# Performance work log

Hardware: AMD Instinct MI355X
Metric: run time of the kernel (lower is better)

Reference implementation:

```python
import jax, jax.numpy as jnp
import numpy as np

EMBED_DIM = 1024
NUM_HEADS = 16
HEAD_DIM = EMBED_DIM // NUM_HEADS
SCALE = HEAD_DIM ** -0.5
B, S = 2, 2048


def setup_inputs() -> dict:
    key = jax.random.key(0)
    ks = jax.random.split(key, 11)
    lim = 1.0 / np.sqrt(EMBED_DIM)
    def lin(kw, kb):
        W = jax.random.uniform(kw, (EMBED_DIM, EMBED_DIM), jnp.float32, -lim, lim)
        b = jax.random.uniform(kb, (EMBED_DIM,), jnp.float32, -lim, lim)
        return W, b
    Wq, bq = lin(ks[0], ks[1])
    Wk, bk = lin(ks[2], ks[3])
    Wv, bv = lin(ks[4], ks[5])
    Wo, bo = lin(ks[6], ks[7])
    query = jax.random.normal(ks[8], (B, S, EMBED_DIM), jnp.float32)
    key_t = jax.random.normal(ks[9], (B, S, EMBED_DIM), jnp.float32)
    value = jax.random.normal(ks[10], (B, S, EMBED_DIM), jnp.float32)
    return {"query": query, "key": key_t, "value": value,
            "Wq": Wq, "bq": bq, "Wk": Wk, "bk": bk,
            "Wv": Wv, "bv": bv, "Wo": Wo, "bo": bo}


def reference(query, key, value, Wq, bq, Wk, bk, Wv, bv, Wo, bo):
    # 'flash' path with attn_mask=None == full softmax attention (chunking is
    # only an execution schedule; per-chunk softmax is over the full key axis).
    b, s, _ = query.shape
    def heads(x, W, bias):
        y = x @ W.T + bias                      # [b, s, E]
        return y.reshape(b, s, NUM_HEADS, HEAD_DIM).transpose(0, 2, 1, 3)  # [b, h, s, d]
    q = heads(query, Wq, bq)
    k = heads(key, Wk, bk)
    v = heads(value, Wv, bv)
    scores = jnp.einsum('bhqd,bhkd->bhqk', q, k) * SCALE
    attn = jax.nn.softmax(scores, axis=-1)
    out = jnp.einsum('bhqk,bhkd->bhqd', attn, v)
    out = out.transpose(0, 2, 1, 3).reshape(b, s, EMBED_DIM)
    return out @ Wo.T + bo
```

## Files before the change

### kernel.cpp

```cpp
#include <hip/hip_runtime.h>

typedef unsigned short u16;
typedef unsigned int u32;
typedef __attribute__((ext_vector_type(8))) __bf16 bf16x8;
typedef __attribute__((ext_vector_type(4))) float f32x4;
typedef __attribute__((ext_vector_type(16))) float f32x16;
typedef __attribute__((ext_vector_type(4))) unsigned short u16x4;
typedef __attribute__((ext_vector_type(8))) unsigned short u16x8;
typedef __attribute__((ext_vector_type(4))) unsigned int u32x4;

#define DEV static __device__ __forceinline__

DEV void async_copy16(const void* g, void* l) {
  __builtin_amdgcn_global_load_lds((const __attribute__((address_space(1))) void*)g,
                                   (__attribute__((address_space(3))) void*)l, 16, 0, 0);
}
DEV float b2f(u16 s) { union { unsigned u; float f; } v; v.u = ((unsigned)s) << 16; return v.f; }
DEV u16 f2b(float f) {
  union { float f; unsigned u; } v; v.f = f;
  unsigned r = v.u + 0x7FFFu + ((v.u >> 16) & 1u);
  return (u16)(r >> 16);
}
DEV u32 pack2bf(float a, float b) {
  u32 ua = __float_as_uint(a) + 0x8000u;
  u32 ub = __float_as_uint(b) + 0x8000u;
  return __builtin_amdgcn_perm(ub, ua, 0x07060302u);
}
DEV int wave_detect_bf16(const unsigned* q, int lane) {
  const unsigned w = q[lane & 63];
  const unsigned e = (w >> 7) & 0xFFu;
  const bool inr = (e >= 100u && e <= 132u);
  return (__popcll(__ballot(inr)) >= 48) ? 1 : 0;
}

#define MFMA(a, b, c) __builtin_amdgcn_mfma_f32_16x16x32_bf16((a), (b), (c), 0, 0, 0)
#define MFMA32(a, b, c) __builtin_amdgcn_mfma_f32_32x32x16_bf16((a), (b), (c), 0, 0, 0)

__global__ void convert_inputs(
    const void* s0, const void* s1, const void* s2,
    const void* s3, const void* s4, const void* s5, const void* s6,
    const void* s7, const void* s8, const void* s9, const void* s10,
    u16* __restrict__ d0, u16* __restrict__ d1, u16* __restrict__ d2,
    u16* __restrict__ d3, u16* __restrict__ d4, u16* __restrict__ d5, u16* __restrict__ d6,
    float* __restrict__ e7, float* __restrict__ e8, float* __restrict__ e9, float* __restrict__ e10)
{
  const int bi = blockIdx.y;
  const void* src = nullptr; u16* db = nullptr; float* df = nullptr; int n = 0;
  switch (bi) {
    case 0:  src = s0;  db = d0; n = 4194304; break;
    case 1:  src = s1;  db = d1; n = 4194304; break;
    case 2:  src = s2;  db = d2; n = 4194304; break;
    case 3:  src = s3;  db = d3; n = 1048576; break;
    case 4:  src = s4;  db = d4; n = 1048576; break;
    case 5:  src = s5;  db = d5; n = 1048576; break;
    case 6:  src = s6;  db = d6; n = 1048576; break;
    case 7:  src = s7;  df = e7; n = 1024; break;
    case 8:  src = s8;  df = e8; n = 1024; break;
    case 9:  src = s9;  df = e9; n = 1024; break;
    default: src = s10; df = e10; n = 1024; break;
  }
  const int isbf = wave_detect_bf16((const unsigned*)s0, threadIdx.x);
  const int stride = gridDim.x * 256 * 8;
  for (int i = (blockIdx.x * 256 + threadIdx.x) * 8; i < n; i += stride) {
    if (db) {
      u16x8 v;
      if (isbf) {
        v = *(const u16x8*)((const u16*)src + i);
      } else {
        const f32x4* sf = (const f32x4*)((const float*)src + i);
        const f32x4 x0 = sf[0], x1 = sf[1];
#pragma unroll
        for (int j = 0; j < 4; ++j) { v[j] = f2b(x0[j]); v[4 + j] = f2b(x1[j]); }
      }
      *(u16x8*)(db + i) = v;
    } else {
#pragma unroll
      for (int j = 0; j < 8; ++j) {
        float x = isbf ? b2f(((const u16*)src)[i + j]) : ((const float*)src)[i + j];
        df[i + j] = x;
      }
    }
  }
}

__global__ __launch_bounds__(256, 3)
void gemm_qkv(const u16* __restrict__ X0, const u16* __restrict__ X1, const u16* __restrict__ X2,
              const u16* __restrict__ W0, const u16* __restrict__ W1, const u16* __restrict__ W2,
              const float* __restrict__ B0, const float* __restrict__ B1, const float* __restrict__ B2,
              u16* __restrict__ Y0, u16* __restrict__ Y1, u16* __restrict__ Y2,
              float* __restrict__ Yf, const unsigned* __restrict__ qdet, int mode0)
{
  __shared__ __align__(16) u16 smem[17408];
  u16* As = smem;
  u16* Bs = smem + 8192;

  const int z = blockIdx.z;
  const u16* X  = (z == 0) ? X0 : ((z == 1) ? X1 : X2);
  const u16* W  = (z == 0) ? W0 : ((z == 1) ? W1 : W2);
  const float* Bi = (z == 0) ? B0 : ((z == 1) ? B1 : B2);
  u16* Y        = (z == 0) ? Y0 : ((z == 1) ? Y1 : Y2);
  const int mode = mode0 ? mode0 : z;

  const int t = threadIdx.x, wave = t >> 6, lane = t & 63;
  const int lane15 = lane & 15, quad = lane >> 4, l7 = lane15 & 7;
  const int m0 = blockIdx.y * 128, n0 = blockIdx.x * 128;

  const int srow = lane >> 3;
  const int schunk = (lane & 7) ^ srow;
  const u16* gA = X + (size_t)(m0 + wave * 32 + srow) * 1024 + schunk * 8;
  const u16* gB = W + (size_t)(n0 + wave * 32 + srow) * 1024 + schunk * 8;
  u16* lA = &As[wave * 32 * 64];
  u16* lB = &Bs[wave * 32 * 64];

  f32x4 acc[4][4];
#pragma unroll
  for (int i = 0; i < 4; ++i)
#pragma unroll
    for (int j = 0; j < 4; ++j) acc[i][j] = (f32x4){0.f, 0.f, 0.f, 0.f};

  const int wr = wave >> 1, wc = wave & 1;

  for (int k0 = 0; k0 < 1024; k0 += 64) {
#pragma unroll
    for (int r = 0; r < 4; ++r) async_copy16(gA + (size_t)r * 8 * 1024, lA + r * 8 * 64);
#pragma unroll
    for (int r = 0; r < 4; ++r) async_copy16(gB + (size_t)r * 8 * 1024, lB + r * 8 * 64);
    gA += 64; gB += 64;
    __syncthreads();

#pragma unroll
    for (int kk = 0; kk < 2; ++kk) {
      bf16x8 af[4], bfv[4];
#pragma unroll
      for (int mt = 0; mt < 4; ++mt)
        af[mt] = *(const bf16x8*)&As[(wr * 64 + mt * 16 + lane15) * 64 + ((kk * 4 + quad) ^ l7) * 8];
#pragma unroll
      for (int nt = 0; nt < 4; ++nt)
        bfv[nt] = *(const bf16x8*)&Bs[(wc * 64 + nt * 16 + lane15) * 64 + ((kk * 4 + quad) ^ l7) * 8];
#pragma unroll
      for (int mt = 0; mt < 4; ++mt)
#pragma unroll
        for (int nt = 0; nt < 4; ++nt)
          acc[mt][nt] = MFMA(af[mt], bfv[nt], acc[mt][nt]);
    }
    __syncthreads();
  }

  const float qscale = 0.125f * 1.44269504088896340736f;

  if (mode == 2) {
    u16* T2 = smem;
    __syncthreads();
#pragma unroll
    for (int mt = 0; mt < 4; ++mt) {
      const int sl_base = wr * 64 + mt * 16 + quad * 4;
#pragma unroll
      for (int nt = 0; nt < 4; ++nt) {
        const int nn = wc * 64 + nt * 16 + lane15;
        const float bias_v = Bi[n0 + nn];
#pragma unroll
        for (int r = 0; r < 4; ++r)
          T2[nn * 136 + sl_base + r] = f2b(acc[mt][nt][r] + bias_v);
      }
    }
    __syncthreads();
    const size_t grow0 = (size_t)(m0 >> 11) * 1024 + n0;
    const int col0 = m0 & 2047;
#pragma unroll
    for (int i = 0; i < 8; ++i) {
      const int id = i * 256 + t;
      const int row = id >> 4, ch = id & 15;
      *(u16x8*)&Y[(grow0 + row) * 2048 + col0 + ch * 8] = *(const u16x8*)&T2[row * 136 + ch * 8];
    }
    return;
  }

  if (mode == 3) {
    const int outbf = wave_detect_bf16(qdet, lane);
    if (outbf) {
      u16* T2 = smem;
      __syncthreads();
#pragma unroll
      for (int mt = 0; mt < 4; ++mt) {
        const int ml = wr * 64 + mt * 16 + quad * 4;
#pragma unroll
        for (int nt = 0; nt < 4; ++nt) {
          const int nl = wc * 64 + nt * 16 + lane15;
          const float bias_v = Bi[n0 + nl];
#pragma unroll
          for (int r = 0; r < 4; ++r)
            T2[(ml + r) * 136 + nl] = f2b(acc[mt][nt][r] + bias_v);
        }
      }
      __syncthreads();
#pragma unroll
      for (int i = 0; i < 8; ++i) {
        const int id = i * 256 + t;
        const int row = id >> 4, ch = id & 15;
        *(u16x8*)&Y[(size_t)(m0 + row) * 1024 + n0 + ch * 8] = *(const u16x8*)&T2[row * 136 + ch * 8];
      }
    } else {
#pragma unroll
      for (int mt = 0; mt < 4; ++mt) {
        const int m_base = m0 + wr * 64 + mt * 16 + quad * 4;
#pragma unroll
        for (int nt = 0; nt < 4; ++nt) {
          const int n = n0 + wc * 64 + nt * 16 + lane15;
          const float bias_v = Bi[n];
#pragma unroll
          for (int r = 0; r < 4; ++r)
            Yf[(size_t)(m_base + r) * 1024 + n] = acc[mt][nt][r] + bias_v;
        }
      }
    }
    return;
  }

  u16* T3 = smem;
  __syncthreads();
#pragma unroll
  for (int mt = 0; mt < 4; ++mt) {
    const int sl = wr * 64 + mt * 16 + quad * 4;
#pragma unroll
    for (int nt = 0; nt < 4; ++nt) {
      const int d_loc = nt * 16 + lane15;
      const float bias_v = Bi[n0 + wc * 64 + d_loc];
#pragma unroll
      for (int r = 0; r < 4; ++r) {
        float v = acc[mt][nt][r] + bias_v;
        if (mode == 0) v *= qscale;
        T3[wc * 8704 + (sl + r) * 68 + d_loc] = f2b(v);
      }
    }
  }
  __syncthreads();
  const int bb = m0 >> 11, s0 = m0 & 2047, h0 = n0 >> 6;
#pragma unroll
  for (int i = 0; i < 8; ++i) {
    const int id = i * 256 + t;
    const int hh = id >> 10, row = (id >> 3) & 127, ch = id & 7;
    *(u16x8*)&Y[(((size_t)bb * 16 + h0 + hh) * 2048 + s0 + row) * 64 + ch * 8] =
        *(const u16x8*)&T3[hh * 8704 + row * 68 + ch * 8];
  }
}

__global__ __launch_bounds__(256, 2)
void flash_attn(const u16* __restrict__ Qs, const u16* __restrict__ Ks,
                const u16* __restrict__ Vt, u16* __restrict__ AO)
{
  __shared__ __align__(16) u16 smem[32768];

  const int t = threadIdx.x, w = t >> 6, lane = t & 63;
  const int l31 = lane & 31, half = lane >> 5;
  const int lin = blockIdx.y * 16 + blockIdx.x;
  const int bh = lin & 31;
  const int q0 = (lin >> 5) * 128;

  const u16* Qb = Qs + ((size_t)bh * 2048 + q0) * 64;
  const u16* Kb = Ks + (size_t)bh * 2048 * 64;
  const u16* Vb = Vt + (size_t)bh * 64 * 2048;

  const int krow = lane >> 3;
  const int kchunk = (lane & 7) ^ krow;
  const int vrow = lane >> 4;
  const int vcb = lane & 15;

#pragma unroll
  for (int r = 0; r < 4; ++r)
    async_copy16(Qb + (size_t)(r * 32 + w * 8 + krow) * 64 + kchunk * 8,
                 &smem[(r * 32 + w * 8) * 64]);
  __syncthreads();
  const int qrow = w * 32 + l31;
  bf16x8 bq[4];
#pragma unroll
  for (int ks = 0; ks < 4; ++ks)
    bq[ks] = *(const bf16x8*)&smem[qrow * 64 + (((ks * 2 + half) ^ (qrow & 7))) * 8];

  {
    u16* Kn = smem + 16384;
    u16* Vn = smem + 24576;
#pragma unroll
    for (int r = 0; r < 4; ++r)
      async_copy16(Kb + (size_t)(r * 32 + w * 8 + krow) * 64 + kchunk * 8,
                   &Kn[(r * 32 + w * 8) * 64]);
#pragma unroll
    for (int r = 0; r < 4; ++r) {
      const int d = r * 16 + w * 4 + vrow;
      async_copy16(Vb + (size_t)d * 2048 + (vcb ^ (d & 7)) * 8,
                   &Vn[(r * 16 + w * 4) * 128]);
    }
  }
  __syncthreads();

  f32x16 acc[2];
#pragma unroll
  for (int dt = 0; dt < 2; ++dt)
#pragma unroll
    for (int i = 0; i < 16; ++i) acc[dt][i] = 0.f;
  float lpart = 0.f;

  for (int kt = 0; kt < 16; ++kt) {
    u16* Kc = smem + ((kt + 1) & 1) * 16384;
    u16* Vc = Kc + 8192;
    if (kt < 15) {
      u16* Kn = smem + (kt & 1) * 16384;
      u16* Vn = Kn + 8192;
#pragma unroll
      for (int r = 0; r < 4; ++r)
        async_copy16(Kb + (size_t)((kt + 1) * 128 + r * 32 + w * 8 + krow) * 64 + kchunk * 8,
                     &Kn[(r * 32 + w * 8) * 64]);
#pragma unroll
      for (int r = 0; r < 4; ++r) {
        const int d = r * 16 + w * 4 + vrow;
        async_copy16(Vb + (size_t)d * 2048 + (kt + 1) * 128 + (vcb ^ (d & 7)) * 8,
                     &Vn[(r * 16 + w * 4) * 128]);
      }
    }

#pragma unroll
    for (int ktile = 0; ktile < 4; ++ktile) {
      const int key = ktile * 32 + l31;
      f32x16 st;
#pragma unroll
      for (int i = 0; i < 16; ++i) st[i] = 0.f;
#pragma unroll
      for (int ks = 0; ks < 4; ++ks) {
        const bf16x8 ak = *(const bf16x8*)&Kc[key * 64 + (((ks * 2 + half) ^ (key & 7))) * 8];
        st = MFMA32(ak, bq[ks], st);
      }
      float p[16];
      float ts = 0.f;
#pragma unroll
      for (int i = 0; i < 16; ++i) { p[i] = __builtin_amdgcn_exp2f(st[i]); ts += p[i]; }
      lpart += ts;
      u32 pk0[4], pk1[4];
#pragma unroll
      for (int rq = 0; rq < 4; ++rq) {
        pk0[rq] = pack2bf(p[4 * rq + 0], p[4 * rq + 1]);
        pk1[rq] = pack2bf(p[4 * rq + 2], p[4 * rq + 3]);
      }
#pragma unroll
      for (int s2 = 0; s2 < 2; ++s2) {
        const u32 own0 = half ? pk0[2 * s2 + 1] : pk0[2 * s2];
        const u32 own1 = half ? pk1[2 * s2 + 1] : pk1[2 * s2];
        const u32 snd0 = half ? pk0[2 * s2] : pk0[2 * s2 + 1];
        const u32 snd1 = half ? pk1[2 * s2] : pk1[2 * s2 + 1];
        const u32 rcv0 = (u32)__shfl_xor((int)snd0, 32);
        const u32 rcv1 = (u32)__shfl_xor((int)snd1, 32);
        u32x4 bp;
        bp[0] = half ? rcv0 : own0;
        bp[1] = half ? rcv1 : own1;
        bp[2] = half ? own0 : rcv0;
        bp[3] = half ? own1 : rcv1;
        const bf16x8 bfrag = __builtin_bit_cast(bf16x8, bp);
#pragma unroll
        for (int dt = 0; dt < 2; ++dt) {
          const int d = dt * 32 + l31;
          const int c = ktile * 4 + s2 * 2 + half;
          const bf16x8 av = *(const bf16x8*)&Vc[d * 128 + ((c ^ (d & 7))) * 8];
          acc[dt] = MFMA32(av, bfrag, acc[dt]);
        }
      }
    }
    __syncthreads();
  }

  const float lfull = lpart + __shfl_xor(lpart, 32);
  const float rl = 1.0f / lfull;

  u16* T = smem;
#pragma unroll
  for (int dt = 0; dt < 2; ++dt)
#pragma unroll
    for (int rq = 0; rq < 4; ++rq) {
      u16x4 v4;
#pragma unroll
      for (int o = 0; o < 4; ++o) v4[o] = f2b(acc[dt][rq * 4 + o] * rl);
      *(u16x4*)&T[qrow * 72 + dt * 32 + rq * 8 + half * 4] = v4;
    }
  __syncthreads();

  const int b = bh >> 4, h = bh & 15;
#pragma unroll
  for (int i = 0; i < 4; ++i) {
    const int id = i * 256 + t;
    const int row = id >> 3, ch = id & 7;
    *(u16x8*)&AO[((size_t)b * 2048 + q0 + row) * 1024 + h * 64 + ch * 8] =
        *(const u16x8*)&T[row * 72 + ch * 8];
  }
}

extern "C" void kernel_launch(void* const* d_in, const int* in_sizes, int n_in,
                              void* d_out, int out_size, void* d_ws, size_t ws_size,
                              hipStream_t stream)
{
  const void* query = d_in[0];
  const void* key_  = d_in[1];
  const void* value = d_in[2];
  const void* Wq = d_in[3]; const void* bq = d_in[4];
  const void* Wk = d_in[5]; const void* bk = d_in[6];
  const void* Wv = d_in[7]; const void* bv = d_in[8];
  const void* Wo = d_in[9]; const void* bo = d_in[10];

  u16* ws = (u16*)d_ws;
  u16* Qs  = ws;
  u16* Ks  = Qs + 4194304;
  u16* Vt  = Ks + 4194304;
  u16* AO  = Vt + 4194304;
  u16* Xq  = AO + 4194304;
  u16* Xk  = Xq + 4194304;
  u16* Xv  = Xk + 4194304;
  u16* Wqc = Xv + 4194304;
  u16* Wkc = Wqc + 1048576;
  u16* Wvc = Wkc + 1048576;
  u16* Woc = Wvc + 1048576;
  float* Bc = (float*)(Woc + 1048576);

  convert_inputs<<<dim3(128, 11), 256, 0, stream>>>(
      query, key_, value, Wq, Wk, Wv, Wo, bq, bk, bv, bo,
      Xq, Xk, Xv, Wqc, Wkc, Wvc, Woc,
      Bc, Bc + 1024, Bc + 2048, Bc + 3072);

  gemm_qkv<<<dim3(8, 32, 3), 256, 0, stream>>>(Xq, Xk, Xv, Wqc, Wkc, Wvc,
                                               Bc, Bc + 1024, Bc + 2048,
                                               Qs, Ks, Vt, nullptr,
                                               (const unsigned*)query, 0);
  flash_attn<<<dim3(16, 32), 256, 0, stream>>>(Qs, Ks, Vt, AO);
  gemm_qkv<<<dim3(8, 32, 1), 256, 0, stream>>>(AO, AO, AO, Woc, Woc, Woc,
                                               Bc + 3072, Bc + 3072, Bc + 3072,
                                               (u16*)d_out, (u16*)d_out, (u16*)d_out,
                                               (float*)d_out, (const unsigned*)query, 3);
}
```

Before: 233.9 us.

## Fuse fp32-to-bf16 input conversion into GEMM loads and batch QK^T MFMAs

Removes the separate convert_inputs kernel. The QKV and output GEMMs now read fp32 activations and weights directly, converting them to bf16 in registers while staging into swizzled LDS. This avoids writing and re-reading bf16 copies of the inputs and saves a kernel launch. The cost is that the async global-to-LDS copy is replaced by synchronous vector loads plus conversion in the GEMM main loop. Flash attention is also restructured to issue all four key-tile score MFMAs before the exp/pack phase, exposing more ILP at the cost of more live registers.

```diff
diff --git a/kernel.cpp b/kernel.cpp
--- a/kernel.cpp
+++ b/kernel.cpp
@@ -32,61 +32,17 @@
   const bool inr = (e >= 100u && e <= 132u);
   return (__popcll(__ballot(inr)) >= 48) ? 1 : 0;
 }
+DEV float loadb(const void* B, int n, int isbf) {
+  return isbf ? b2f(((const u16*)B)[n]) : ((const float*)B)[n];
+}
 
 #define MFMA(a, b, c) __builtin_amdgcn_mfma_f32_16x16x32_bf16((a), (b), (c), 0, 0, 0)
 #define MFMA32(a, b, c) __builtin_amdgcn_mfma_f32_32x32x16_bf16((a), (b), (c), 0, 0, 0)
 
-__global__ void convert_inputs(
-    const void* s0, const void* s1, const void* s2,
-    const void* s3, const void* s4, const void* s5, const void* s6,
-    const void* s7, const void* s8, const void* s9, const void* s10,
-    u16* __restrict__ d0, u16* __restrict__ d1, u16* __restrict__ d2,
-    u16* __restrict__ d3, u16* __restrict__ d4, u16* __restrict__ d5, u16* __restrict__ d6,
-    float* __restrict__ e7, float* __restrict__ e8, float* __restrict__ e9, float* __restrict__ e10)
-{
-  const int bi = blockIdx.y;
-  const void* src = nullptr; u16* db = nullptr; float* df = nullptr; int n = 0;
-  switch (bi) {
-    case 0:  src = s0;  db = d0; n = 4194304; break;
-    case 1:  src = s1;  db = d1; n = 4194304; break;
-    case 2:  src = s2;  db = d2; n = 4194304; break;
-    case 3:  src = s3;  db = d3; n = 1048576; break;
-    case 4:  src = s4;  db = d4; n = 1048576; break;
-    case 5:  src = s5;  db = d5; n = 1048576; break;
-    case 6:  src = s6;  db = d6; n = 1048576; break;
-    case 7:  src = s7;  df = e7; n = 1024; break;
-    case 8:  src = s8;  df = e8; n = 1024; break;
-    case 9:  src = s9;  df = e9; n = 1024; break;
-    default: src = s10; df = e10; n = 1024; break;
-  }
-  const int isbf = wave_detect_bf16((const unsigned*)s0, threadIdx.x);
-  const int stride = gridDim.x * 256 * 8;
-  for (int i = (blockIdx.x * 256 + threadIdx.x) * 8; i < n; i += stride) {
-    if (db) {
-      u16x8 v;
-      if (isbf) {
-        v = *(const u16x8*)((const u16*)src + i);
-      } else {
-        const f32x4* sf = (const f32x4*)((const float*)src + i);
-        const f32x4 x0 = sf[0], x1 = sf[1];
-#pragma unroll
-        for (int j = 0; j < 4; ++j) { v[j] = f2b(x0[j]); v[4 + j] = f2b(x1[j]); }
-      }
-      *(u16x8*)(db + i) = v;
-    } else {
-#pragma unroll
-      for (int j = 0; j < 8; ++j) {
-        float x = isbf ? b2f(((const u16*)src)[i + j]) : ((const float*)src)[i + j];
-        df[i + j] = x;
-      }
-    }
-  }
-}
-
 __global__ __launch_bounds__(256, 3)
-void gemm_qkv(const u16* __restrict__ X0, const u16* __restrict__ X1, const u16* __restrict__ X2,
-              const u16* __restrict__ W0, const u16* __restrict__ W1, const u16* __restrict__ W2,
-              const float* __restrict__ B0, const float* __restrict__ B1, const float* __restrict__ B2,
+void gemm_qkv(const void* X0, const void* X1, const void* X2,
+              const void* W0, const void* W1, const void* W2,
+              const void* B0, const void* B1, const void* B2,
               u16* __restrict__ Y0, u16* __restrict__ Y1, u16* __restrict__ Y2,
               float* __restrict__ Yf, const unsigned* __restrict__ qdet, int mode0)
 {
@@ -95,23 +51,31 @@
   u16* Bs = smem + 8192;
 
   const int z = blockIdx.z;
-  const u16* X  = (z == 0) ? X0 : ((z == 1) ? X1 : X2);
-  const u16* W  = (z == 0) ? W0 : ((z == 1) ? W1 : W2);
-  const float* Bi = (z == 0) ? B0 : ((z == 1) ? B1 : B2);
-  u16* Y        = (z == 0) ? Y0 : ((z == 1) ? Y1 : Y2);
+  const void* X = (z == 0) ? X0 : ((z == 1) ? X1 : X2);
+  const void* W = (z == 0) ? W0 : ((z == 1) ? W1 : W2);
+  const void* Bi = (z == 0) ? B0 : ((z == 1) ? B1 : B2);
+  u16* Y = (z == 0) ? Y0 : ((z == 1) ? Y1 : Y2);
   const int mode = mode0 ? mode0 : z;
 
   const int t = threadIdx.x, wave = t >> 6, lane = t & 63;
   const int lane15 = lane & 15, quad = lane >> 4, l7 = lane15 & 7;
   const int m0 = blockIdx.y * 128, n0 = blockIdx.x * 128;
 
+  const int isbf = wave_detect_bf16(qdet, lane);
+  const int abf = (mode0 == 3) ? 1 : isbf;
+
   const int srow = lane >> 3;
   const int schunk = (lane & 7) ^ srow;
-  const u16* gA = X + (size_t)(m0 + wave * 32 + srow) * 1024 + schunk * 8;
-  const u16* gB = W + (size_t)(n0 + wave * 32 + srow) * 1024 + schunk * 8;
+  const u16* gA16 = (const u16*)X + (size_t)(m0 + wave * 32 + srow) * 1024 + schunk * 8;
+  const u16* gB16 = (const u16*)W + (size_t)(n0 + wave * 32 + srow) * 1024 + schunk * 8;
   u16* lA = &As[wave * 32 * 64];
   u16* lB = &Bs[wave * 32 * 64];
 
+  const float* XF = (const float*)X;
+  const float* WF = (const float*)W;
+  const int rrow = lane >> 4;
+  const int fj = lane & 15, fjc = fj >> 1, fjh = fj & 1, fj4 = fj * 4;
+
   f32x4 acc[4][4];
 #pragma unroll
   for (int i = 0; i < 4; ++i)
@@ -121,11 +85,36 @@
   const int wr = wave >> 1, wc = wave & 1;
 
   for (int k0 = 0; k0 < 1024; k0 += 64) {
-#pragma unroll
-    for (int r = 0; r < 4; ++r) async_copy16(gA + (size_t)r * 8 * 1024, lA + r * 8 * 64);
-#pragma unroll
-    for (int r = 0; r < 4; ++r) async_copy16(gB + (size_t)r * 8 * 1024, lB + r * 8 * 64);
-    gA += 64; gB += 64;
+    if (abf) {
+#pragma unroll
+      for (int r = 0; r < 4; ++r) async_copy16(gA16 + (size_t)r * 8 * 1024, lA + r * 8 * 64);
+      gA16 += 64;
+    } else {
+#pragma unroll
+      for (int op = 0; op < 8; ++op) {
+        const int lrow = wave * 32 + op * 4 + rrow;
+        const f32x4 x = *(const f32x4*)&XF[(size_t)(m0 + lrow) * 1024 + k0 + fj4];
+        u16x4 v;
+#pragma unroll
+        for (int c = 0; c < 4; ++c) v[c] = f2b(x[c]);
+        *(u16x4*)&As[lrow * 64 + (fjc ^ (lrow & 7)) * 8 + fjh * 4] = v;
+      }
+    }
+    if (isbf) {
+#pragma unroll
+      for (int r = 0; r < 4; ++r) async_copy16(gB16 + (size_t)r * 8 * 1024, lB + r * 8 * 64);
+      gB16 += 64;
+    } else {
+#pragma unroll
+      for (int op = 0; op < 8; ++op) {
+        const int lrow = wave * 32 + op * 4 + rrow;
+        const f32x4 x = *(const f32x4*)&WF[(size_t)(n0 + lrow) * 1024 + k0 + fj4];
+        u16x4 v;
+#pragma unroll
+        for (int c = 0; c < 4; ++c) v[c] = f2b(x[c]);
+        *(u16x4*)&Bs[lrow * 64 + (fjc ^ (lrow & 7)) * 8 + fjh * 4] = v;
+      }
+    }
     __syncthreads();
 
 #pragma unroll
@@ -157,7 +146,7 @@
 #pragma unroll
       for (int nt = 0; nt < 4; ++nt) {
         const int nn = wc * 64 + nt * 16 + lane15;
-        const float bias_v = Bi[n0 + nn];
+        const float bias_v = loadb(Bi, n0 + nn, isbf);
 #pragma unroll
         for (int r = 0; r < 4; ++r)
           T2[nn * 136 + sl_base + r] = f2b(acc[mt][nt][r] + bias_v);
@@ -176,8 +165,7 @@
   }
 
   if (mode == 3) {
-    const int outbf = wave_detect_bf16(qdet, lane);
-    if (outbf) {
+    if (isbf) {
       u16* T2 = smem;
       __syncthreads();
 #pragma unroll
@@ -186,7 +174,7 @@
 #pragma unroll
         for (int nt = 0; nt < 4; ++nt) {
           const int nl = wc * 64 + nt * 16 + lane15;
-          const float bias_v = Bi[n0 + nl];
+          const float bias_v = loadb(Bi, n0 + nl, 1);
 #pragma unroll
           for (int r = 0; r < 4; ++r)
             T2[(ml + r) * 136 + nl] = f2b(acc[mt][nt][r] + bias_v);
@@ -206,7 +194,7 @@
 #pragma unroll
         for (int nt = 0; nt < 4; ++nt) {
           const int n = n0 + wc * 64 + nt * 16 + lane15;
-          const float bias_v = Bi[n];
+          const float bias_v = loadb(Bi, n, 0);
 #pragma unroll
           for (int r = 0; r < 4; ++r)
             Yf[(size_t)(m_base + r) * 1024 + n] = acc[mt][nt][r] + bias_v;
@@ -224,7 +212,7 @@
 #pragma unroll
     for (int nt = 0; nt < 4; ++nt) {
       const int d_loc = nt * 16 + lane15;
-      const float bias_v = Bi[n0 + wc * 64 + d_loc];
+      const float bias_v = loadb(Bi, n0 + wc * 64 + d_loc, isbf);
 #pragma unroll
       for (int r = 0; r < 4; ++r) {
         float v = acc[mt][nt][r] + bias_v;
@@ -317,34 +305,45 @@
       }
     }
 
+    f32x16 st[4];
+#pragma unroll
+    for (int ktile = 0; ktile < 4; ++ktile)
+#pragma unroll
+      for (int i = 0; i < 16; ++i) st[ktile][i] = 0.f;
+#pragma unroll
+    for (int ks = 0; ks < 4; ++ks)
+#pragma unroll
+      for (int ktile = 0; ktile < 4; ++ktile) {
+        const int key = ktile * 32 + l31;
+        const bf16x8 ak = *(const bf16x8*)&Kc[key * 64 + (((ks * 2 + half) ^ (key & 7))) * 8];
+        st[ktile] = MFMA32(ak, bq[ks], st[ktile]);
+      }
+
+    u32 pk0[4][4], pk1[4][4];
 #pragma unroll
     for (int ktile = 0; ktile < 4; ++ktile) {
-      const int key = ktile * 32 + l31;
-      f32x16 st;
-#pragma unroll
-      for (int i = 0; i < 16; ++i) st[i] = 0.f;
-#pragma unroll
-      for (int ks = 0; ks < 4; ++ks) {
-        const bf16x8 ak = *(const bf16x8*)&Kc[key * 64 + (((ks * 2 + half) ^ (key & 7))) * 8];
-        st = MFMA32(ak, bq[ks], st);
-      }
-      float p[16];
       float ts = 0.f;
 #pragma unroll
-      for (int i = 0; i < 16; ++i) { p[i] = __builtin_amdgcn_exp2f(st[i]); ts += p[i]; }
+      for (int rq = 0; rq < 4; ++rq) {
+        const float p0 = __builtin_amdgcn_exp2f(st[ktile][4 * rq + 0]);
+        const float p1 = __builtin_amdgcn_exp2f(st[ktile][4 * rq + 1]);
+        const float p2 = __builtin_amdgcn_exp2f(st[ktile][4 * rq + 2]);
+        const float p3 = __builtin_amdgcn_exp2f(st[ktile][4 * rq + 3]);
+        ts += (p0 + p1) + (p2 + p3);
+        pk0[ktile][rq] = pack2bf(p0, p1);
+        pk1[ktile][rq] = pack2bf(p2, p3);
+      }
       lpart += ts;
-      u32 pk0[4], pk1[4];
-#pragma unroll
-      for (int rq = 0; rq < 4; ++rq) {
-        pk0[rq] = pack2bf(p[4 * rq + 0], p[4 * rq + 1]);
-        pk1[rq] = pack2bf(p[4 * rq + 2], p[4 * rq + 3]);
-      }
+    }
+
+#pragma unroll
+    for (int ktile = 0; ktile < 4; ++ktile)
 #pragma unroll
       for (int s2 = 0; s2 < 2; ++s2) {
-        const u32 own0 = half ? pk0[2 * s2 + 1] : pk0[2 * s2];
-        const u32 own1 = half ? pk1[2 * s2 + 1] : pk1[2 * s2];
-        const u32 snd0 = half ? pk0[2 * s2] : pk0[2 * s2 + 1];
-        const u32 snd1 = half ? pk1[2 * s2] : pk1[2 * s2 + 1];
+        const u32 own0 = half ? pk0[ktile][2 * s2 + 1] : pk0[ktile][2 * s2];
+        const u32 own1 = half ? pk1[ktile][2 * s2 + 1] : pk1[ktile][2 * s2];
+        const u32 snd0 = half ? pk0[ktile][2 * s2] : pk0[ktile][2 * s2 + 1];
+        const u32 snd1 = half ? pk1[ktile][2 * s2] : pk1[ktile][2 * s2 + 1];
         const u32 rcv0 = (u32)__shfl_xor((int)snd0, 32);
         const u32 rcv1 = (u32)__shfl_xor((int)snd1, 32);
         u32x4 bp;
@@ -361,7 +360,6 @@
           acc[dt] = MFMA32(av, bfrag, acc[dt]);
         }
       }
-    }
     __syncthreads();
   }
 
@@ -407,27 +405,13 @@
   u16* Ks  = Qs + 4194304;
   u16* Vt  = Ks + 4194304;
   u16* AO  = Vt + 4194304;
-  u16* Xq  = AO + 4194304;
-  u16* Xk  = Xq + 4194304;
-  u16* Xv  = Xk + 4194304;
-  u16* Wqc = Xv + 4194304;
-  u16* Wkc = Wqc + 1048576;
-  u16* Wvc = Wkc + 1048576;
-  u16* Woc = Wvc + 1048576;
-  float* Bc = (float*)(Woc + 1048576);
-
-  convert_inputs<<<dim3(128, 11), 256, 0, stream>>>(
-      query, key_, value, Wq, Wk, Wv, Wo, bq, bk, bv, bo,
-      Xq, Xk, Xv, Wqc, Wkc, Wvc, Woc,
-      Bc, Bc + 1024, Bc + 2048, Bc + 3072);
-
-  gemm_qkv<<<dim3(8, 32, 3), 256, 0, stream>>>(Xq, Xk, Xv, Wqc, Wkc, Wvc,
-                                               Bc, Bc + 1024, Bc + 2048,
-                                               Qs, Ks, Vt, nullptr,
+
+  gemm_qkv<<<dim3(8, 32, 3), 256, 0, stream>>>(query, key_, value, Wq, Wk, Wv,
+                                               bq, bk, bv, Qs, Ks, Vt, nullptr,
                                                (const unsigned*)query, 0);
   flash_attn<<<dim3(16, 32), 256, 0, stream>>>(Qs, Ks, Vt, AO);
-  gemm_qkv<<<dim3(8, 32, 1), 256, 0, stream>>>(AO, AO, AO, Woc, Woc, Woc,
-                                               Bc + 3072, Bc + 3072, Bc + 3072,
+  gemm_qkv<<<dim3(8, 32, 1), 256, 0, stream>>>(AO, AO, AO, Wo, Wo, Wo,
+                                               bo, bo, bo,
                                                (u16*)d_out, (u16*)d_out, (u16*)d_out,
                                                (float*)d_out, (const unsigned*)query, 3);
 }
```

Result: slower. 348.6 us (+49.0%).

## Double-buffer QKV GEMM tiles and batch attention QK MFMAs before softmax

Applied to the files above, without the earlier changes.

The QKV projection GEMM now keeps two LDS stages and prefetches the next K-block with async copies while the current one is consumed. Shared memory grows to 64 KB and the occupancy hint drops from 3 to 2 blocks per CU. In the attention kernel, the QK^T MFMAs for all four key tiles are issued together before the exp/pack/PV stage, which gives more independent MFMA work to hide latency at the cost of more live registers. The extra syncthreads before the epilogues are removed because the loop already ends with a barrier.

```diff
diff --git a/kernel.cpp b/kernel.cpp
--- a/kernel.cpp
+++ b/kernel.cpp
@@ -83,16 +83,14 @@
   }
 }
 
-__global__ __launch_bounds__(256, 3)
+__global__ __launch_bounds__(256, 2)
 void gemm_qkv(const u16* __restrict__ X0, const u16* __restrict__ X1, const u16* __restrict__ X2,
               const u16* __restrict__ W0, const u16* __restrict__ W1, const u16* __restrict__ W2,
               const float* __restrict__ B0, const float* __restrict__ B1, const float* __restrict__ B2,
               u16* __restrict__ Y0, u16* __restrict__ Y1, u16* __restrict__ Y2,
               float* __restrict__ Yf, const unsigned* __restrict__ qdet, int mode0)
 {
-  __shared__ __align__(16) u16 smem[17408];
-  u16* As = smem;
-  u16* Bs = smem + 8192;
+  __shared__ __align__(16) u16 smem[32768];
 
   const int z = blockIdx.z;
   const u16* X  = (z == 0) ? X0 : ((z == 1) ? X1 : X2);
@@ -109,8 +107,6 @@
   const int schunk = (lane & 7) ^ srow;
   const u16* gA = X + (size_t)(m0 + wave * 32 + srow) * 1024 + schunk * 8;
   const u16* gB = W + (size_t)(n0 + wave * 32 + srow) * 1024 + schunk * 8;
-  u16* lA = &As[wave * 32 * 64];
-  u16* lB = &Bs[wave * 32 * 64];
 
   f32x4 acc[4][4];
 #pragma unroll
@@ -119,15 +115,31 @@
     for (int j = 0; j < 4; ++j) acc[i][j] = (f32x4){0.f, 0.f, 0.f, 0.f};
 
   const int wr = wave >> 1, wc = wave & 1;
-
-  for (int k0 = 0; k0 < 1024; k0 += 64) {
+  const int woff = wave * 32 * 64;
+
+  {
+    u16* lA = &smem[woff];
+    u16* lB = &smem[8192 + woff];
 #pragma unroll
     for (int r = 0; r < 4; ++r) async_copy16(gA + (size_t)r * 8 * 1024, lA + r * 8 * 64);
 #pragma unroll
     for (int r = 0; r < 4; ++r) async_copy16(gB + (size_t)r * 8 * 1024, lB + r * 8 * 64);
-    gA += 64; gB += 64;
-    __syncthreads();
-
+  }
+  __syncthreads();
+
+  for (int kb = 0; kb < 16; ++kb) {
+    const int cur = kb & 1, nxt = cur ^ 1;
+    if (kb < 15) {
+      const size_t ko = (size_t)(kb + 1) * 64;
+      u16* lA = &smem[nxt * 16384 + woff];
+      u16* lB = &smem[nxt * 16384 + 8192 + woff];
+#pragma unroll
+      for (int r = 0; r < 4; ++r) async_copy16(gA + ko + (size_t)r * 8 * 1024, lA + r * 8 * 64);
+#pragma unroll
+      for (int r = 0; r < 4; ++r) async_copy16(gB + ko + (size_t)r * 8 * 1024, lB + r * 8 * 64);
+    }
+    const u16* As = &smem[cur * 16384];
+    const u16* Bs = &smem[cur * 16384 + 8192];
 #pragma unroll
     for (int kk = 0; kk < 2; ++kk) {
       bf16x8 af[4], bfv[4];
@@ -150,7 +162,6 @@
 
   if (mode == 2) {
     u16* T2 = smem;
-    __syncthreads();
 #pragma unroll
     for (int mt = 0; mt < 4; ++mt) {
       const int sl_base = wr * 64 + mt * 16 + quad * 4;
@@ -179,7 +190,6 @@
     const int outbf = wave_detect_bf16(qdet, lane);
     if (outbf) {
       u16* T2 = smem;
-      __syncthreads();
 #pragma unroll
       for (int mt = 0; mt < 4; ++mt) {
         const int ml = wr * 64 + mt * 16 + quad * 4;
@@ -217,7 +227,6 @@
   }
 
   u16* T3 = smem;
-  __syncthreads();
 #pragma unroll
   for (int mt = 0; mt < 4; ++mt) {
     const int sl = wr * 64 + mt * 16 + quad * 4;
@@ -317,34 +326,45 @@
       }
     }
 
+    f32x16 st[4];
+#pragma unroll
+    for (int ktile = 0; ktile < 4; ++ktile)
+#pragma unroll
+      for (int i = 0; i < 16; ++i) st[ktile][i] = 0.f;
+#pragma unroll
+    for (int ks = 0; ks < 4; ++ks)
+#pragma unroll
+      for (int ktile = 0; ktile < 4; ++ktile) {
+        const int key = ktile * 32 + l31;
+        const bf16x8 ak = *(const bf16x8*)&Kc[key * 64 + (((ks * 2 + half) ^ (key & 7))) * 8];
+        st[ktile] = MFMA32(ak, bq[ks], st[ktile]);
+      }
+
+    u32 pk0[4][4], pk1[4][4];
 #pragma unroll
     for (int ktile = 0; ktile < 4; ++ktile) {
-      const int key = ktile * 32 + l31;
-      f32x16 st;
-#pragma unroll
-      for (int i = 0; i < 16; ++i) st[i] = 0.f;
-#pragma unroll
-      for (int ks = 0; ks < 4; ++ks) {
-        const bf16x8 ak = *(const bf16x8*)&Kc[key * 64 + (((ks * 2 + half) ^ (key & 7))) * 8];
-        st = MFMA32(ak, bq[ks], st);
-      }
-      float p[16];
       float ts = 0.f;
 #pragma unroll
-      for (int i = 0; i < 16; ++i) { p[i] = __builtin_amdgcn_exp2f(st[i]); ts += p[i]; }
+      for (int rq = 0; rq < 4; ++rq) {
+        const float p0 = __builtin_amdgcn_exp2f(st[ktile][4 * rq + 0]);
+        const float p1 = __builtin_amdgcn_exp2f(st[ktile][4 * rq + 1]);
+        const float p2 = __builtin_amdgcn_exp2f(st[ktile][4 * rq + 2]);
+        const float p3 = __builtin_amdgcn_exp2f(st[ktile][4 * rq + 3]);
+        ts += (p0 + p1) + (p2 + p3);
+        pk0[ktile][rq] = pack2bf(p0, p1);
+        pk1[ktile][rq] = pack2bf(p2, p3);
+      }
       lpart += ts;
-      u32 pk0[4], pk1[4];
-#pragma unroll
-      for (int rq = 0; rq < 4; ++rq) {
-        pk0[rq] = pack2bf(p[4 * rq + 0], p[4 * rq + 1]);
-        pk1[rq] = pack2bf(p[4 * rq + 2], p[4 * rq + 3]);
-      }
+    }
+
+#pragma unroll
+    for (int ktile = 0; ktile < 4; ++ktile)
 #pragma unroll
       for (int s2 = 0; s2 < 2; ++s2) {
-        const u32 own0 = half ? pk0[2 * s2 + 1] : pk0[2 * s2];
-        const u32 own1 = half ? pk1[2 * s2 + 1] : pk1[2 * s2];
-        const u32 snd0 = half ? pk0[2 * s2] : pk0[2 * s2 + 1];
-        const u32 snd1 = half ? pk1[2 * s2] : pk1[2 * s2 + 1];
+        const u32 own0 = half ? pk0[ktile][2 * s2 + 1] : pk0[ktile][2 * s2];
+        const u32 own1 = half ? pk1[ktile][2 * s2 + 1] : pk1[ktile][2 * s2];
+        const u32 snd0 = half ? pk0[ktile][2 * s2] : pk0[ktile][2 * s2 + 1];
+        const u32 snd1 = half ? pk1[ktile][2 * s2] : pk1[ktile][2 * s2 + 1];
         const u32 rcv0 = (u32)__shfl_xor((int)snd0, 32);
         const u32 rcv1 = (u32)__shfl_xor((int)snd1, 32);
         u32x4 bp;
@@ -361,7 +381,6 @@
           acc[dt] = MFMA32(av, bfrag, acc[dt]);
         }
       }
-    }
     __syncthreads();
   }
 
```

New measurement: 233.9 us. Within noise of the previous version (-0.0%).
